# Kernel optimization log

Hardware: AMD Instinct MI355X
Metric: run time of the kernel (lower is better)

The kernel has to match this reference:

```python
import jax, jax.numpy as jnp
import numpy as np

EMBED = 128
HEADS = 8
B, S = 2, 2048


def setup_inputs() -> dict:
    key = jax.random.key(0)
    ks = jax.random.split(key, 9)
    scale = 1.0 / np.sqrt(EMBED)
    return {
        "values": jax.random.normal(ks[0], (B, S, EMBED), dtype=jnp.float32),
        "keys": jax.random.normal(ks[1], (B, S, EMBED), dtype=jnp.float32),
        "query": jax.random.normal(ks[2], (B, S, EMBED), dtype=jnp.float32),
        "mask": jax.random.randint(ks[3], (B, 1, S, S), 0, 2, dtype=jnp.int32),
        # torch Linear weights: (out_features, in_features)
        "Wv": jax.random.normal(ks[4], (EMBED * HEADS, EMBED), dtype=jnp.float32) * scale,
        "Wk": jax.random.normal(ks[5], (EMBED * HEADS, EMBED), dtype=jnp.float32) * scale,
        "Wq": jax.random.normal(ks[6], (EMBED * HEADS, EMBED), dtype=jnp.float32) * scale,
        "Wu": jax.random.normal(ks[7], (EMBED, EMBED * HEADS), dtype=jnp.float32) * scale,
        "bu": jax.random.normal(ks[8], (EMBED,), dtype=jnp.float32) * 0.01,
    }


def reference(values, keys, query, mask, Wv, Wk, Wq, Wu, bu):
    n, vl, e = values.shape
    kl = keys.shape[1]
    ql = query.shape[1]
    h = Wv.shape[0] // e

    v = (values @ Wv.T).reshape(n, vl, h, e)   # (n, k, h, d)
    k = (keys @ Wk.T).reshape(n, kl, h, e)
    q = (query @ Wq.T).reshape(n, ql, h, e)

    dot = jnp.einsum("nqhd,nkhd->nhqk", q, k)  # (n, h, q, k)
    dot = jnp.where(mask == 0, jnp.float32(-1e20), dot)
    attn = jax.nn.softmax(dot / jnp.sqrt(jnp.float32(e)), axis=3)

    out = jnp.einsum("nhqk,nkhd->nqhd", attn, v).reshape(n, ql, h * e)
    return out @ Wu.T + bu
```

## Files before the change

### kernel.cpp

```cpp
#include <hip/hip_runtime.h>

typedef unsigned short u16;
typedef unsigned int u32;
typedef unsigned long long u64;
typedef __attribute__((ext_vector_type(8))) short bf16x8;
typedef __attribute__((ext_vector_type(4))) float f32x4;
typedef __attribute__((ext_vector_type(16))) float f32x16;
typedef __attribute__((ext_vector_type(4))) u32 u32x4;
typedef __attribute__((ext_vector_type(4))) int i32x4;

#define GLOAD16(gp, lp)                                                        \
  __builtin_amdgcn_global_load_lds(                                            \
      (__attribute__((address_space(1))) void*)(gp),                           \
      (__attribute__((address_space(3))) void*)(lp), 16, 0, 0)

#if __has_builtin(__builtin_amdgcn_exp2f)
#define EXP2(x) __builtin_amdgcn_exp2f(x)
#else
#define EXP2(x) __expf(0.6931471805599453f * (x))
#endif

#define Z16                                                                    \
  { 0.f, 0.f, 0.f, 0.f, 0.f, 0.f, 0.f, 0.f, 0.f, 0.f, 0.f, 0.f, 0.f, 0.f,     \
    0.f, 0.f }

__device__ __forceinline__ u16 f2bf(float f) {
  u32 u = __builtin_bit_cast(u32, f);
  u += 0x7FFFu + ((u >> 16) & 1u);
  return (u16)(u >> 16);
}

__device__ __forceinline__ float bf2f(short s) {
  return __builtin_bit_cast(float, (u32)(u16)s << 16);
}

__device__ __forceinline__ u32 cvtpk(float lo, float hi) {
  u32 r;
  asm("v_cvt_pk_bf16_f32 %0, %1, %2" : "=v"(r) : "v"(lo), "v"(hi));
  return r;
}

__device__ __forceinline__ void plswap(u32& a, u32& b) {
  asm volatile("v_permlane32_swap_b32 %0, %1" : "+v"(a), "+v"(b));
}

__device__ __forceinline__ f32x4 MFMA(bf16x8 a, bf16x8 b, f32x4 c) {
  return __builtin_amdgcn_mfma_f32_16x16x32_bf16(a, b, c, 0, 0, 0);
}
__device__ __forceinline__ f32x16 MFMA32(bf16x8 a, bf16x8 b, f32x16 c) {
  return __builtin_amdgcn_mfma_f32_32x32x16_bf16(a, b, c, 0, 0, 0);
}

__device__ __forceinline__ u32x4 cvt8(f32x4 a, f32x4 b) {
  u32x4 o;
  o[0] = cvtpk(a[0], a[1]);
  o[1] = cvtpk(a[2], a[3]);
  o[2] = cvtpk(b[0], b[1]);
  o[3] = cvtpk(b[2], b[3]);
  return o;
}

__global__ __launch_bounds__(256) void kmask(const int* __restrict__ mask,
                                             const float* __restrict__ bu,
                                             u64* __restrict__ pm64,
                                             float* __restrict__ outp) {
  const int blk = blockIdx.x, tid = threadIdx.x;
  if (blk < 512) {
    int idx = blk * 256 + tid;
    f32x4 bv = *(const f32x4*)(bu + ((idx * 4) & 127));
    *((f32x4*)outp + idx) = bv;
  }
  const u32 W = blk * 256 + tid;
  const u32 half = W & 1, q = (W >> 1) & 2047, t = (W >> 12) & 31, b = W >> 17;
  const int* src = mask + ((size_t)b * 2048 + q) * 2048 + t * 64 + half * 32;
  i32x4 v[8];
#pragma unroll
  for (int j = 0; j < 8; j++) v[j] = *(const i32x4*)(src + j * 4);
  u32 wbits = 0;
#pragma unroll
  for (int j = 0; j < 8; j++) {
    if (v[j][0]) wbits |= 1u << (j * 4 + 0);
    if (v[j][1]) wbits |= 1u << (j * 4 + 1);
    if (v[j][2]) wbits |= 1u << (j * 4 + 2);
    if (v[j][3]) wbits |= 1u << (j * 4 + 3);
  }
  ((u32*)pm64)[W] = wbits;
}

__global__ __launch_bounds__(256) void kproj(
    const float* __restrict__ Xq, const float* __restrict__ Xk,
    const float* __restrict__ Xv, const float* __restrict__ Wqf,
    const float* __restrict__ Wkf, const float* __restrict__ Wvf,
    u16* __restrict__ Qh, u16* __restrict__ Kh, u16* __restrict__ Vt) {
  __shared__ alignas(128) u16 ldsA[128 * 128];
  __shared__ alignas(128) u16 ldsB[64 * 128];
  const int z = blockIdx.z;
  const int mt = blockIdx.x, nt = blockIdx.y;
  const int tid = threadIdx.x;
  const float* X = z == 0 ? Xq : (z == 1 ? Xk : Xv);
  const float* W = z == 0 ? Wqf : (z == 1 ? Wkf : Wvf);
  const int w = tid >> 6, lane = tid & 63;
  const int lo = lane & 15, hi = lane >> 4;

#pragma unroll
  for (int i = 0; i < 8; i++) {
    int cid = i * 256 + tid;
    int r = cid >> 4, c = cid & 15;
    const float* src = X + (size_t)(mt * 128 + r) * 128 + c * 8;
    f32x4 a = *(const f32x4*)src;
    f32x4 b = *(const f32x4*)(src + 4);
    *(u32x4*)(ldsA + r * 128 + (c ^ (r & 7)) * 8) = cvt8(a, b);
  }
#pragma unroll
  for (int i = 0; i < 4; i++) {
    int cid = i * 256 + tid;
    int r = cid >> 4, c = cid & 15;
    const float* src = W + (size_t)(nt * 64 + r) * 128 + c * 8;
    f32x4 a = *(const f32x4*)src;
    f32x4 b = *(const f32x4*)(src + 4);
    *(u32x4*)(ldsB + r * 128 + (c ^ (r & 7)) * 8) = cvt8(a, b);
  }
  __syncthreads();

  const int wm = (w >> 1) * 64, wn = (w & 1) * 32;
  f32x4 zero = {0.f, 0.f, 0.f, 0.f};
  f32x4 acc[4][2];
#pragma unroll
  for (int a = 0; a < 4; a++)
#pragma unroll
    for (int b2 = 0; b2 < 2; b2++) acc[a][b2] = zero;

#pragma unroll
  for (int t = 0; t < 4; t++) {
    bf16x8 af[4], bfr[2];
#pragma unroll
    for (int fm = 0; fm < 4; fm++) {
      int r = wm + fm * 16 + lo;
      int ch = (t * 4 + hi) ^ (r & 7);
      af[fm] = *(const bf16x8*)(ldsA + r * 128 + ch * 8);
    }
#pragma unroll
    for (int fn = 0; fn < 2; fn++) {
      int r = wn + fn * 16 + lo;
      int ch = (t * 4 + hi) ^ (r & 7);
      bfr[fn] = *(const bf16x8*)(ldsB + r * 128 + ch * 8);
    }
#pragma unroll
    for (int fm = 0; fm < 4; fm++)
#pragma unroll
      for (int fn = 0; fn < 2; fn++)
        acc[fm][fn] = MFMA(af[fm], bfr[fn], acc[fm][fn]);
  }

  if (z < 2) {
    u16* dst = z == 0 ? Qh : Kh;
    const float scale = z == 0 ? 0.12753103392461437f : 1.0f;
#pragma unroll
    for (int fm = 0; fm < 4; fm++)
#pragma unroll
      for (int fn = 0; fn < 2; fn++) {
        int n = nt * 64 + wn + fn * 16 + lo;
        int h = n >> 7, d = n & 127;
#pragma unroll
        for (int j = 0; j < 4; j++) {
          int m = mt * 128 + wm + fm * 16 + hi * 4 + j;
          int b = m >> 11, s = m & 2047;
          dst[(((size_t)(b * 8 + h) * 2048) + s) * 128 + d] =
              f2bf(acc[fm][fn][j] * scale);
        }
      }
  } else {
    typedef __attribute__((ext_vector_type(4))) u16 u16x4t;
#pragma unroll
    for (int fm = 0; fm < 4; fm++)
#pragma unroll
      for (int fn = 0; fn < 2; fn++) {
        int n = nt * 64 + wn + fn * 16 + lo;
        int h = n >> 7, d = n & 127;
        int m0 = mt * 128 + wm + fm * 16 + hi * 4;
        int b = m0 >> 11, s0 = m0 & 2047;
        u16x4t pk4;
#pragma unroll
        for (int j = 0; j < 4; j++) pk4[j] = f2bf(acc[fm][fn][j]);
        *(u16x4t*)(Vt + ((size_t)(b * 8 + h) * 128 + d) * 2048 + s0) = pk4;
      }
  }
}

__global__ __launch_bounds__(256, 2) void kattn(
    const u16* __restrict__ Qh, const u16* __restrict__ Kh,
    const u16* __restrict__ Vt, const u64* __restrict__ pm64,
    u16* __restrict__ OP, float2* __restrict__ ML, int ntiles) {
  __shared__ alignas(128) u16 ldsK[2][64 * 128];
  __shared__ alignas(128) u16 ldsV[2][128 * 64];
  const int bh = blockIdx.x;
  const int half = blockIdx.y;
  const int qblk = blockIdx.z;
  const int b = bh >> 3, h = bh & 7;
  const int ktbase = half * ntiles;
  u16* outO = OP + (size_t)half * 4194304;
  const float CSH = 24.0f;

  const int tid = threadIdx.x, w = tid >> 6, lane = tid & 63;
  const int lo5 = lane & 31, h5 = lane >> 5;
  const int q0w = qblk * 128 + w * 32;
  const int q = q0w + lo5;
  const u16* Qb = Qh + (size_t)bh * 262144;
  const u16* Kb = Kh + (size_t)bh * 262144;
  const u16* Vb = Vt + (size_t)bh * 262144;
  const u64* pmb = pm64 + ((size_t)b << 16);

  int kgo[4], vgo[4], slo[4];
#pragma unroll
  for (int i = 0; i < 4; i++) {
    int off = (w * 4 + i) * 1024 + lane * 16;
    slo[i] = off;
    { int r = off >> 8, c = (off >> 4) & 15, gs = c ^ (r & 7);
      kgo[i] = r * 128 + gs * 8; }
    { int d = off >> 7, c = (off >> 4) & 7, gs = c ^ (d & 7);
      vgo[i] = d * 2048 + gs * 8; }
  }
  int kro[8], vro[4];
#pragma unroll
  for (int ds = 0; ds < 8; ds++)
    kro[ds] = lo5 * 256 + (((ds * 2 + h5) ^ (lo5 & 7)) * 16);
#pragma unroll
  for (int g2 = 0; g2 < 4; g2++)
    vro[g2] = lo5 * 128 + (((g2 * 2 + h5) ^ (lo5 & 7)) * 16);

  bf16x8 vones;
  {
    u32 onesw = (lo5 == 0) ? 0x3F803F80u : 0u;
    u32x4 t = {onesw, onesw, onesw, onesw};
    vones = __builtin_bit_cast(bf16x8, t);
  }

#define STAGE(kt, bb)                                                          \
  do {                                                                         \
    const int k0_ = (kt) * 64;                                                 \
    _Pragma("unroll") for (int i = 0; i < 4; i++)                              \
        GLOAD16(Kb + (size_t)k0_ * 128 + kgo[i],                               \
                (char*)ldsK + (bb) * 16384 + slo[i]);                          \
    _Pragma("unroll") for (int i = 0; i < 4; i++)                              \
        GLOAD16(Vb + k0_ + vgo[i], (char*)ldsV + (bb) * 16384 + slo[i]);       \
  } while (0)

  bf16x8 qb[8];
#pragma unroll
  for (int ds = 0; ds < 8; ds++)
    qb[ds] = *(const bf16x8*)(Qb + (size_t)q * 128 + ds * 16 + h5 * 8);

  asm volatile("" ::: "memory");
  STAGE(ktbase, 0);
  asm volatile("" ::: "memory");

  f32x16 o0 = Z16, o1 = Z16, o2 = Z16, o3 = Z16, o4 = Z16;

  for (int t = 0; t < ntiles; ++t) {
    const int bb = t & 1;
    __builtin_amdgcn_s_barrier();
    u64 mw = pmb[((size_t)(ktbase + t) << 11) + q];
    if (t + 1 < ntiles) {
      STAGE(ktbase + t + 1, bb ^ 1);
      asm volatile("s_waitcnt vmcnt(9)" ::: "memory");
    } else {
      asm volatile("s_waitcnt vmcnt(1)" ::: "memory");
    }
    __builtin_amdgcn_sched_barrier(0);
    __builtin_amdgcn_s_barrier();
    const char* Kt = (const char*)ldsK + bb * 16384;
    const char* Vl = (const char*)ldsV + bb * 16384;

    f32x16 s0v = Z16, s1v = Z16;
    __builtin_amdgcn_s_setprio(1);
#pragma unroll
    for (int ds = 0; ds < 8; ds++) {
      bf16x8 ka0 = *(const bf16x8*)(Kt + kro[ds]);
      bf16x8 ka1 = *(const bf16x8*)(Kt + kro[ds] + 8192);
      s0v = MFMA32(ka0, qb[ds], s0v);
      s1v = MFMA32(ka1, qb[ds], s1v);
    }
    __builtin_amdgcn_s_setprio(0);

    const u32 mw0 = (u32)mw, mw1 = (u32)(mw >> 32);
#pragma unroll
    for (int r = 0; r < 16; r++) {
      const int rowr = (r & 3) + 8 * (r >> 2) + 4 * h5;
      float p0 = EXP2(s0v[r] - CSH);
      float p1 = EXP2(s1v[r] - CSH);
      p0 = ((mw0 >> rowr) & 1u) ? p0 : 0.0f;
      p1 = ((mw1 >> rowr) & 1u) ? p1 : 0.0f;
      s0v[r] = p0;
      s1v[r] = p1;
    }

    bf16x8 pa[4];
#pragma unroll
    for (int kk = 0; kk < 2; kk++)
#pragma unroll
      for (int sl = 0; sl < 2; sl++) {
        const int rb = sl * 8;
        u32 W0, W1, W2, W3;
        if (kk == 0) {
          W0 = cvtpk(s0v[rb + 0], s0v[rb + 1]);
          W1 = cvtpk(s0v[rb + 2], s0v[rb + 3]);
          W2 = cvtpk(s0v[rb + 4], s0v[rb + 5]);
          W3 = cvtpk(s0v[rb + 6], s0v[rb + 7]);
        } else {
          W0 = cvtpk(s1v[rb + 0], s1v[rb + 1]);
          W1 = cvtpk(s1v[rb + 2], s1v[rb + 3]);
          W2 = cvtpk(s1v[rb + 4], s1v[rb + 5]);
          W3 = cvtpk(s1v[rb + 6], s1v[rb + 7]);
        }
        plswap(W0, W2);
        plswap(W1, W3);
        u32x4 tt = {W0, W1, W2, W3};
        pa[kk * 2 + sl] = __builtin_bit_cast(bf16x8, tt);
      }

    __builtin_amdgcn_s_setprio(1);
#pragma unroll
    for (int gsl = 0; gsl < 4; gsl++) {
      bf16x8 vb0 = *(const bf16x8*)(Vl + vro[gsl] + 0 * 4096);
      bf16x8 vb1 = *(const bf16x8*)(Vl + vro[gsl] + 1 * 4096);
      bf16x8 vb2 = *(const bf16x8*)(Vl + vro[gsl] + 2 * 4096);
      bf16x8 vb3 = *(const bf16x8*)(Vl + vro[gsl] + 3 * 4096);
      o0 = MFMA32(pa[gsl], vb0, o0);
      o1 = MFMA32(pa[gsl], vb1, o1);
      o2 = MFMA32(pa[gsl], vb2, o2);
      o3 = MFMA32(pa[gsl], vb3, o3);
      o4 = MFMA32(pa[gsl], vones, o4);
    }
    __builtin_amdgcn_s_setprio(0);
  }
#undef STAGE

  float linv4[16];
#pragma unroll
  for (int r = 0; r < 16; r++) {
    float lr_ = __shfl(o4[r], h5 * 32);
    linv4[r] = lr_ > 0.f ? 1.0f / lr_ : 0.f;
  }
#pragma unroll
  for (int r = 0; r < 16; r++) {
    const int rowr = (r & 3) + 8 * (r >> 2) + 4 * h5;
    const float fr = linv4[r];
    const size_t base =
        ((size_t)(b * 2048 + q0w + rowr)) * 1024 + h * 128 + lo5;
    outO[base + 0] = f2bf(o0[r] * fr);
    outO[base + 32] = f2bf(o1[r] * fr);
    outO[base + 64] = f2bf(o2[r] * fr);
    outO[base + 96] = f2bf(o3[r] * fr);
  }
  if (lo5 == 0) {
#pragma unroll
    for (int r = 0; r < 16; r++) {
      const int rowr = (r & 3) + 8 * (r >> 2) + 4 * h5;
      ML[((size_t)half << 15) + ((size_t)bh << 11) + q0w + rowr] =
          make_float2(CSH, o4[r]);
    }
  }
}

__global__ __launch_bounds__(256) void koutf(
    const u16* __restrict__ OP, const float2* __restrict__ ML,
    const float* __restrict__ Wuf, float* __restrict__ out, int nsplit) {
  __shared__ alignas(128) u16 ldsA[64 * 128];
  __shared__ alignas(128) u16 ldsW[128 * 128];
  const int mt = blockIdx.x;
  const int kc = blockIdx.y;
  const int tid = threadIdx.x, w = tid >> 6, lane = tid & 63;
  const int lo = lane & 15, hi = lane >> 4;
  f32x4 zero = {0.f, 0.f, 0.f, 0.f};
  f32x4 acc[8];
#pragma unroll
  for (int fn = 0; fn < 8; fn++) acc[fn] = zero;

  for (int ks = 0; ks < 2; ++ks) {
    const int h = kc * 2 + ks;
    const int k0 = h * 128;
#pragma unroll
    for (int i = 0; i < 4; i++) {
      int cid = i * 256 + tid;
      int r = cid >> 4, c = cid & 15;
      int m = mt * 64 + r, b = m >> 11, q = m & 2047;
      size_t off = (size_t)m * 1024 + k0 + c * 8;
      bf16x8 x = *(const bf16x8*)(OP + off);
      u32x4 ow;
      if (nsplit == 2) {
        bf16x8 y = *(const bf16x8*)(OP + 4194304 + off);
        size_t mli = (((size_t)(b << 3) + h) << 11) + q;
        float2 A = ML[mli];
        float2 Bv = ML[32768 + mli];
        float mm = fmaxf(A.x, Bv.x);
        float w1 = A.y * EXP2(A.x - mm);
        float w2 = Bv.y * EXP2(Bv.x - mm);
        float inv = 1.0f / (w1 + w2);
        w1 *= inv;
        w2 *= inv;
        float f[8];
#pragma unroll
        for (int j = 0; j < 8; j++) f[j] = w1 * bf2f(x[j]) + w2 * bf2f(y[j]);
        ow[0] = cvtpk(f[0], f[1]);
        ow[1] = cvtpk(f[2], f[3]);
        ow[2] = cvtpk(f[4], f[5]);
        ow[3] = cvtpk(f[6], f[7]);
      } else {
        ow = __builtin_bit_cast(u32x4, x);
      }
      *(u32x4*)(ldsA + r * 128 + (c ^ (r & 7)) * 8) = ow;
    }
#pragma unroll
    for (int i = 0; i < 8; i++) {
      int cid = i * 256 + tid;
      int r = cid >> 4, c = cid & 15;
      const float* src = Wuf + (size_t)r * 1024 + k0 + c * 8;
      f32x4 a = *(const f32x4*)src;
      f32x4 bq = *(const f32x4*)(src + 4);
      *(u32x4*)(ldsW + r * 128 + (c ^ (r & 7)) * 8) = cvt8(a, bq);
    }
    __syncthreads();
    __builtin_amdgcn_s_setprio(1);
#pragma unroll
    for (int t = 0; t < 4; t++) {
      int ra = w * 16 + lo, cha = (t * 4 + hi) ^ (ra & 7);
      bf16x8 af = *(const bf16x8*)(ldsA + ra * 128 + cha * 8);
#pragma unroll
      for (int fn = 0; fn < 8; fn++) {
        int rb = fn * 16 + lo, chb = (t * 4 + hi) ^ (rb & 7);
        bf16x8 bf_ = *(const bf16x8*)(ldsW + rb * 128 + chb * 8);
        acc[fn] = MFMA(af, bf_, acc[fn]);
      }
    }
    __builtin_amdgcn_s_setprio(0);
    __syncthreads();
  }

#pragma unroll
  for (int fn = 0; fn < 8; fn++) {
    int n = fn * 16 + lo;
#pragma unroll
    for (int j = 0; j < 4; j++) {
      int m = mt * 64 + w * 16 + hi * 4 + j;
      unsafeAtomicAdd(&out[(size_t)m * 128 + n], acc[fn][j]);
    }
  }
}

extern "C" void kernel_launch(void* const* d_in, const int* in_sizes, int n_in,
                              void* d_out, int out_size, void* d_ws,
                              size_t ws_size, hipStream_t stream) {
  const float* values = (const float*)d_in[0];
  const float* keys = (const float*)d_in[1];
  const float* query = (const float*)d_in[2];
  const int* mask = (const int*)d_in[3];
  const float* Wv = (const float*)d_in[4];
  const float* Wk = (const float*)d_in[5];
  const float* Wq = (const float*)d_in[6];
  const float* Wu = (const float*)d_in[7];
  const float* bu = (const float*)d_in[8];

  char* ws = (char*)d_ws;
  u16* QH = (u16*)(ws + 0);
  u16* KH = (u16*)(ws + 8388608);
  u16* VT = (u16*)(ws + 16777216);
  u64* PM64 = (u64*)(ws + 25165824);
  float2* MLb = (float2*)(ws + 26214400);
  u16* OP = (u16*)(ws + 27262976);

  const size_t base = 27262976;
  int nsplit = (ws_size >= base + 2ull * 8388608) ? 2 : 1;
  int ntiles = 32 / nsplit;

  float* out = (float*)d_out;
  kmask<<<1024, 256, 0, stream>>>(mask, bu, PM64, out);
  kproj<<<dim3(32, 16, 3), 256, 0, stream>>>(query, keys, values, Wq, Wk, Wv,
                                             QH, KH, VT);
  kattn<<<dim3(16, nsplit, 16), 256, 0, stream>>>(QH, KH, VT, PM64, OP, MLb,
                                                  ntiles);
  koutf<<<dim3(64, 4), 256, 0, stream>>>(OP, MLb, Wu, out, nsplit);
}
```

Measured before the change: 82.98 us.

## Fold mask packing into projection launch and pre-convert Wu to bf16

```diff
diff --git a/kernel.cpp b/kernel.cpp
--- a/kernel.cpp
+++ b/kernel.cpp
@@ -8,6 +8,7 @@
 typedef __attribute__((ext_vector_type(16))) float f32x16;
 typedef __attribute__((ext_vector_type(4))) u32 u32x4;
 typedef __attribute__((ext_vector_type(4))) int i32x4;
+typedef __attribute__((ext_vector_type(4))) u16 u16x4t;
 
 #define GLOAD16(gp, lp)                                                        \
   __builtin_amdgcn_global_load_lds(                                            \
@@ -60,43 +61,53 @@
   return o;
 }
 
-__global__ __launch_bounds__(256) void kmask(const int* __restrict__ mask,
-                                             const float* __restrict__ bu,
-                                             u64* __restrict__ pm64,
-                                             float* __restrict__ outp) {
-  const int blk = blockIdx.x, tid = threadIdx.x;
-  if (blk < 512) {
-    int idx = blk * 256 + tid;
-    f32x4 bv = *(const f32x4*)(bu + ((idx * 4) & 127));
-    *((f32x4*)outp + idx) = bv;
-  }
-  const u32 W = blk * 256 + tid;
-  const u32 half = W & 1, q = (W >> 1) & 2047, t = (W >> 12) & 31, b = W >> 17;
-  const int* src = mask + ((size_t)b * 2048 + q) * 2048 + t * 64 + half * 32;
-  i32x4 v[8];
-#pragma unroll
-  for (int j = 0; j < 8; j++) v[j] = *(const i32x4*)(src + j * 4);
-  u32 wbits = 0;
-#pragma unroll
-  for (int j = 0; j < 8; j++) {
-    if (v[j][0]) wbits |= 1u << (j * 4 + 0);
-    if (v[j][1]) wbits |= 1u << (j * 4 + 1);
-    if (v[j][2]) wbits |= 1u << (j * 4 + 2);
-    if (v[j][3]) wbits |= 1u << (j * 4 + 3);
-  }
-  ((u32*)pm64)[W] = wbits;
-}
-
 __global__ __launch_bounds__(256) void kproj(
     const float* __restrict__ Xq, const float* __restrict__ Xk,
     const float* __restrict__ Xv, const float* __restrict__ Wqf,
     const float* __restrict__ Wkf, const float* __restrict__ Wvf,
-    u16* __restrict__ Qh, u16* __restrict__ Kh, u16* __restrict__ Vt) {
-  __shared__ alignas(128) u16 ldsA[128 * 128];
-  __shared__ alignas(128) u16 ldsB[64 * 128];
+    const int* __restrict__ mask, const float* __restrict__ bu,
+    const float* __restrict__ Wuf, u16* __restrict__ Qh, u16* __restrict__ Kh,
+    u16* __restrict__ Vt, u64* __restrict__ pm64, u16* __restrict__ Wub16,
+    float* __restrict__ outp) {
   const int z = blockIdx.z;
   const int mt = blockIdx.x, nt = blockIdx.y;
   const int tid = threadIdx.x;
+  if (z == 3) {
+    const int fid = mt + nt * 32;
+    const int idx = fid * 256 + tid;
+    f32x4 bv = *(const f32x4*)(bu + ((idx * 4) & 127));
+    *((f32x4*)outp + idx) = bv;
+    if (idx < 32768) {
+      f32x4 wv4 = *(const f32x4*)(Wuf + (size_t)idx * 4);
+      u16x4t o;
+      o[0] = f2bf(wv4[0]); o[1] = f2bf(wv4[1]);
+      o[2] = f2bf(wv4[2]); o[3] = f2bf(wv4[3]);
+      *(u16x4t*)(Wub16 + (size_t)idx * 4) = o;
+    }
+#pragma unroll
+    for (int j = 0; j < 2; j++) {
+      const u32 W = fid * 512 + j * 256 + tid;
+      const u32 half = W & 1, q = (W >> 1) & 2047, t5 = (W >> 12) & 31,
+                b = W >> 17;
+      const int* src =
+          mask + ((size_t)b * 2048 + q) * 2048 + t5 * 64 + half * 32;
+      i32x4 v[8];
+#pragma unroll
+      for (int k = 0; k < 8; k++) v[k] = *(const i32x4*)(src + k * 4);
+      u32 wbits = 0;
+#pragma unroll
+      for (int k = 0; k < 8; k++) {
+        if (v[k][0]) wbits |= 1u << (k * 4 + 0);
+        if (v[k][1]) wbits |= 1u << (k * 4 + 1);
+        if (v[k][2]) wbits |= 1u << (k * 4 + 2);
+        if (v[k][3]) wbits |= 1u << (k * 4 + 3);
+      }
+      ((u32*)pm64)[W] = wbits;
+    }
+    return;
+  }
+  __shared__ alignas(128) u16 ldsA[128 * 128];
+  __shared__ alignas(128) u16 ldsB[64 * 128];
   const float* X = z == 0 ? Xq : (z == 1 ? Xk : Xv);
   const float* W = z == 0 ? Wqf : (z == 1 ? Wkf : Wvf);
   const int w = tid >> 6, lane = tid & 63;
@@ -170,7 +181,6 @@
         }
       }
   } else {
-    typedef __attribute__((ext_vector_type(4))) u16 u16x4t;
 #pragma unroll
     for (int fm = 0; fm < 4; fm++)
 #pragma unroll
@@ -364,19 +374,26 @@
 
 __global__ __launch_bounds__(256) void koutf(
     const u16* __restrict__ OP, const float2* __restrict__ ML,
-    const float* __restrict__ Wuf, float* __restrict__ out, int nsplit) {
-  __shared__ alignas(128) u16 ldsA[64 * 128];
-  __shared__ alignas(128) u16 ldsW[128 * 128];
+    const u16* __restrict__ Wub16, float* __restrict__ out, int nsplit) {
+  __shared__ alignas(128) u16 ldsA[2][64 * 128];
+  __shared__ alignas(128) u16 ldsW[2][128 * 128];
   const int mt = blockIdx.x;
   const int kc = blockIdx.y;
   const int tid = threadIdx.x, w = tid >> 6, lane = tid & 63;
   const int lo = lane & 15, hi = lane >> 4;
-  f32x4 zero = {0.f, 0.f, 0.f, 0.f};
-  f32x4 acc[8];
-#pragma unroll
-  for (int fn = 0; fn < 8; fn++) acc[fn] = zero;
-
-  for (int ks = 0; ks < 2; ++ks) {
+
+#pragma unroll
+  for (int ks = 0; ks < 2; ks++) {
+    const int k0 = (kc * 2 + ks) * 128;
+#pragma unroll
+    for (int i = 0; i < 8; i++) {
+      int off = (w * 8 + i) * 1024 + lane * 16;
+      int r = off >> 8, c = (off >> 4) & 15, g = c ^ (r & 7);
+      GLOAD16(Wub16 + (size_t)r * 1024 + k0 + g * 8, (char*)ldsW[ks] + off);
+    }
+  }
+#pragma unroll
+  for (int ks = 0; ks < 2; ks++) {
     const int h = kc * 2 + ks;
     const int k0 = h * 128;
 #pragma unroll
@@ -408,33 +425,31 @@
       } else {
         ow = __builtin_bit_cast(u32x4, x);
       }
-      *(u32x4*)(ldsA + r * 128 + (c ^ (r & 7)) * 8) = ow;
-    }
-#pragma unroll
-    for (int i = 0; i < 8; i++) {
-      int cid = i * 256 + tid;
-      int r = cid >> 4, c = cid & 15;
-      const float* src = Wuf + (size_t)r * 1024 + k0 + c * 8;
-      f32x4 a = *(const f32x4*)src;
-      f32x4 bq = *(const f32x4*)(src + 4);
-      *(u32x4*)(ldsW + r * 128 + (c ^ (r & 7)) * 8) = cvt8(a, bq);
-    }
-    __syncthreads();
-    __builtin_amdgcn_s_setprio(1);
+      *(u32x4*)(ldsA[ks] + r * 128 + (c ^ (r & 7)) * 8) = ow;
+    }
+  }
+  __syncthreads();
+
+  f32x4 zero = {0.f, 0.f, 0.f, 0.f};
+  f32x4 acc[8];
+#pragma unroll
+  for (int fn = 0; fn < 8; fn++) acc[fn] = zero;
+  __builtin_amdgcn_s_setprio(1);
+#pragma unroll
+  for (int ks = 0; ks < 2; ks++) {
 #pragma unroll
     for (int t = 0; t < 4; t++) {
       int ra = w * 16 + lo, cha = (t * 4 + hi) ^ (ra & 7);
-      bf16x8 af = *(const bf16x8*)(ldsA + ra * 128 + cha * 8);
+      bf16x8 af = *(const bf16x8*)(ldsA[ks] + ra * 128 + cha * 8);
 #pragma unroll
       for (int fn = 0; fn < 8; fn++) {
         int rb = fn * 16 + lo, chb = (t * 4 + hi) ^ (rb & 7);
-        bf16x8 bf_ = *(const bf16x8*)(ldsW + rb * 128 + chb * 8);
+        bf16x8 bf_ = *(const bf16x8*)(ldsW[ks] + rb * 128 + chb * 8);
         acc[fn] = MFMA(af, bf_, acc[fn]);
       }
     }
-    __builtin_amdgcn_s_setprio(0);
-    __syncthreads();
-  }
+  }
+  __builtin_amdgcn_s_setprio(0);
 
 #pragma unroll
   for (int fn = 0; fn < 8; fn++) {
@@ -466,6 +481,7 @@
   u16* VT = (u16*)(ws + 16777216);
   u64* PM64 = (u64*)(ws + 25165824);
   float2* MLb = (float2*)(ws + 26214400);
+  u16* WUB16 = (u16*)(ws + 26738688);
   u16* OP = (u16*)(ws + 27262976);
 
   const size_t base = 27262976;
@@ -473,10 +489,10 @@
   int ntiles = 32 / nsplit;
 
   float* out = (float*)d_out;
-  kmask<<<1024, 256, 0, stream>>>(mask, bu, PM64, out);
-  kproj<<<dim3(32, 16, 3), 256, 0, stream>>>(query, keys, values, Wq, Wk, Wv,
-                                             QH, KH, VT);
+  kproj<<<dim3(32, 16, 4), 256, 0, stream>>>(query, keys, values, Wq, Wk, Wv,
+                                             mask, bu, Wu, QH, KH, VT, PM64,
+                                             WUB16, out);
   kattn<<<dim3(16, nsplit, 16), 256, 0, stream>>>(QH, KH, VT, PM64, OP, MLb,
                                                   ntiles);
-  koutf<<<dim3(64, 4), 256, 0, stream>>>(OP, MLb, Wu, out, nsplit);
-}
+  koutf<<<dim3(64, 4), 256, 0, stream>>>(OP, MLb, WUB16, out, nsplit);
+}
```

Measured after the change: 80.48 us, median of 2. -3.0%, faster.
